# Kernel tuning notes

Measured on AMD Instinct MI355X. Metric: run time of the kernel, lower is better.

Reference implementation:

```python
import jax, jax.numpy as jnp
import numpy as np

N = 50000        # num_nodes
E = 800000       # num edges (avg degree 16)
IN = 512         # embedding_dim[0]
H = 128          # hidden_dim = embedding_dim[1]
C = 64           # out_dim = n_classes = embedding_dim[-1]
L = 3            # layer_num = len(embedding_dim) - 1


def _lin(k, fan_in, fan_out):
    s = 1.0 / np.sqrt(fan_in)
    k1, k2 = jax.random.split(k)
    W = jax.random.uniform(k1, (fan_in, fan_out), jnp.float32, -s, s)
    b = jax.random.uniform(k2, (fan_out,), jnp.float32, -s, s)
    return W, b


def setup_inputs() -> dict:
    key = jax.random.key(0)
    ks = jax.random.split(key, 12)
    d = {}
    d["x"] = jax.random.normal(ks[0], (N, IN), jnp.float32)
    d["edge_index"] = jax.random.randint(ks[1], (2, E), 0, N)
    # pseudo_mlp: in_dim -> 512 -> 64 -> out_dim
    d["Wp1"], d["bp1"] = _lin(ks[2], IN, 512)
    d["Wp2"], d["bp2"] = _lin(ks[3], 512, 64)
    d["Wp3"], d["bp3"] = _lin(ks[4], 64, C)
    # parsing_mats[0] (only ln=0 is used in learn_soft_edge3), init ones/scaling_factor
    d["parsing0"] = jnp.ones((C, C), jnp.float32) / 2.0 + 0.01 * jax.random.normal(ks[5], (C, C), jnp.float32)
    # GCNConv weights (PyG style: linear without bias, bias added after aggregation)
    d["Wg0"], d["bg0"] = _lin(ks[6], IN, H)
    d["Wg1"], d["bg1"] = _lin(ks[7], H, H)
    d["Wg2"], d["bg2"] = _lin(ks[8], H, H)
    # JK 'cat' -> lin1 input is (layer_num-1)*hidden
    d["Wl1"], d["bl1"] = _lin(ks[9], (L - 1) * H, H)
    d["Wl2"], d["bl2"] = _lin(ks[10], H, C)
    return d


def gcn_conv(x, W, b, edge_index, ew, n):
    """PyG GCNConv with per-edge weight ew, add_self_loops=True (loop weight 1)."""
    xw = x @ W                                           # [N, F_out]
    row, col = edge_index[0], edge_index[1]
    loop = jnp.arange(n)
    row2 = jnp.concatenate([row, loop])
    col2 = jnp.concatenate([col, loop])
    ew2 = jnp.concatenate([ew, jnp.ones((n,), xw.dtype)])
    deg = jax.ops.segment_sum(ew2, col2, num_segments=n)
    dis = jnp.where(deg > 0, jax.lax.rsqrt(deg), 0.0)    # deg^-1/2, inf -> 0
    norm = dis[row2] * ew2 * dis[col2]                   # [E+N]
    out = jax.ops.segment_sum(norm[:, None] * xw[row2], col2, num_segments=n)
    return out + b


def soft_edge_weight(x, edge_index, Wp1, bp1, Wp2, bp2, Wp3, bp3, parsing0):
    """learn_soft_edge3: bilinear form start^T * relu(2*P) * end per edge.
    Original materializes an [E,C,C] outer product then bmm + diagonal; the
    diagonal-sum equals einsum('ek,ed,dk->e', start, end, parsing), computed
    here as a fused small matmul + elementwise reduce (same math)."""
    h = jax.nn.relu(x @ Wp1 + bp1)
    h = jax.nn.relu(h @ Wp2 + bp2)
    logits = h @ Wp3 + bp3                               # [N, C]
    parsing = jax.nn.relu(2.0 * parsing0)                # scaling_factor = 2
    s = logits[edge_index[0]]                            # [E, C] start
    e = logits[edge_index[1]]                            # [E, C] end
    ew = jnp.sum((e @ parsing) * s, axis=-1)             # [E]
    mean = ew.mean()
    var = jnp.var(ew, ddof=1)                            # torch .var() is unbiased
    return (ew - mean) * jnp.sqrt(1e-4 / var) + 1.0


def reference(x, edge_index, Wp1, bp1, Wp2, bp2, Wp3, bp3, parsing0,
              Wg0, bg0, Wg1, bg1, Wg2, bg2, Wl1, bl1, Wl2, bl2):
    n = x.shape[0]
    ew = soft_edge_weight(x, edge_index, Wp1, bp1, Wp2, bp2, Wp3, bp3, parsing0)
    # layer 0
    x1 = jax.nn.relu(gcn_conv(x, Wg0, bg0, edge_index, ew, n))
    xs = [x1]
    # ln = 1 (not last): conv -> relu -> (dropout off in eval) -> append
    x2 = jax.nn.relu(gcn_conv(x1, Wg1, bg1, edge_index, ew, n))
    xs.append(x2)
    # ln = 2 (last layer): computed in original but loop breaks before append;
    # jump(xs) overwrites x, so the last conv's output never reaches the output.
    xj = jnp.concatenate(xs, axis=-1)                    # JK 'cat' -> [N, (L-1)*H]
    out = jax.nn.relu(xj @ Wl1 + bl1)
    out = out @ Wl2 + bl2                                # [N, C]
    return out
```

## Files before the change

### kernel.cpp

```cpp
#include <hip/hip_runtime.h>
#include <hip/hip_bf16.h>
#include <cmath>
#include <cstring>

#define NNODES 50000
#define NEDGES 800000
#define IND    512
#define HD     128
#define CD     64

typedef __bf16 bf16x8 __attribute__((ext_vector_type(8)));
typedef float  f32x4  __attribute__((ext_vector_type(4)));
typedef const __attribute__((address_space(1))) unsigned int* gu32p;
typedef __attribute__((address_space(3))) unsigned int* lu32p;

static const size_t XJ_B   = 0;
static const size_t HID_B  = 25600000;
static const size_t H1_B   = 51200000;
static const size_t XW_B   = 102400000;
static const size_t H2_B   = 115200000;
static const size_t LG_B   = 121600000;
static const size_t PE_B   = 128000000;
static const size_t WT_B   = 134400000;
static const size_t CSRR_B = 135300000;
static const size_t EWC_B  = 138500000;
static const size_t CSRW_B = 141700000;
static const size_t CNT_B  = 144900000;
static const size_t S_B    = 145100000;
static const size_t ZERO_BYTES = 200016;
static const size_t RP_B   = 145100016;
static const size_t WOFF_B = 145300020;
static const size_t INCL_B = 145500020;
static const size_t BSUM_B = 145700020;
static const size_t ST_B   = 145701044;
static const size_t DIS_B  = 145701052;

static const size_t WP1T_O = 0;
static const size_t WG0T_O = 524288;
static const size_t WP2T_O = 655360;
static const size_t WP3T_O = 720896;
static const size_t W2T_O  = 729088;
static const size_t WG1T_O = 737280;
static const size_t WL1T_O = 770048;
static const size_t WL2T_O = 835584;
static const size_t BG1_O  = 851968;
static const size_t BG3_O  = 854528;

struct WD { const float* s; __hip_bfloat16* d; int K; int N; };
struct PrepArgs {
    const float* x; __hip_bfloat16* xb;
    WD w[7];
    int bo[8];
    const float* Wp3; const float* bp3; const float* P0; const float* bp1;
    __hip_bfloat16* W2t; float* bias_g1; float* bias_g3;
};
#define PREP_CAST_BLKS 12500
#define PREP_TP_BLKS   1648
#define PREP_BLKS      (PREP_CAST_BLKS + PREP_TP_BLKS + 20)

__global__ __launch_bounds__(256) void prep_all(PrepArgs a)
{
    int b = blockIdx.x;
    int t = threadIdx.x;
    if (b < PREP_CAST_BLKS) {
        int i = b * 256 + t;
        const float4* p = (const float4*)a.x + (size_t)i * 2;
        float4 u = p[0], v = p[1];
        __hip_bfloat16 o[8] __attribute__((aligned(16)));
        o[0] = __float2bfloat16(u.x); o[1] = __float2bfloat16(u.y);
        o[2] = __float2bfloat16(u.z); o[3] = __float2bfloat16(u.w);
        o[4] = __float2bfloat16(v.x); o[5] = __float2bfloat16(v.y);
        o[6] = __float2bfloat16(v.z); o[7] = __float2bfloat16(v.w);
        *(int4*)(a.xb + (size_t)i * 8) = *(const int4*)o;
        return;
    }
    b -= PREP_CAST_BLKS;
    if (b < PREP_TP_BLKS) {
        int m = 0;
        #pragma unroll
        for (int q = 1; q < 7; q++) if (b >= a.bo[q]) m = q;
        WD d = a.w[m];
        int i = (b - a.bo[m]) * 256 + t;
        if (i < d.K * d.N) {
            int k = i % d.K, n = i / d.K;
            d.d[i] = __float2bfloat16(d.s[(size_t)k * d.N + n]);
        }
        return;
    }
    b -= PREP_TP_BLKS;
    if (b < 16) {
        int i = b * 256 + t;
        int k = i >> 6, n = i & 63;
        float s = 0.f;
        for (int j = 0; j < 64; j++)
            s += a.Wp3[k * 64 + j] * fmaxf(2.f * a.P0[j * 64 + n], 0.f);
        a.W2t[n * 64 + k] = __float2bfloat16(s);
    } else if (b == 16) {
        int n = t;
        if (n < 64) {
            float s = 0.f;
            for (int j = 0; j < 64; j++)
                s += a.bp3[j] * fmaxf(2.f * a.P0[j * 64 + n], 0.f);
            a.bias_g3[n] = a.bp3[n];
            a.bias_g3[64 + n] = s;
        }
    } else {
        int i = (b - 17) * 256 + t;
        if (i < 512) a.bias_g1[i] = a.bp1[i];
        else if (i < 640) a.bias_g1[i] = 0.f;
    }
}

template<int BM, int BN, int WN>
__global__ __launch_bounds__(256) void gemm_mfma(
    const __hip_bfloat16* __restrict__ Ab, int lda,
    const __hip_bfloat16* __restrict__ Bt, int ldb,
    const float* __restrict__ bias,
    void* __restrict__ Cout, int ldc,
    void* __restrict__ Cout2, int ldc2, int splitN,
    int M, int K, int do_relu, int out_bf16)
{
    constexpr int BF = WN / 16;
    constexpr int MI = BM / 32;
    constexpr int APASS = BM / 64;
    constexpr int BPASS = BN / 64;
    __shared__ __bf16 As[2][BM * 32];
    __shared__ __bf16 Bs[2][BN * 32];

    const int NC = gridDim.x, NR = gridDim.y;
    int g = blockIdx.y * NC + blockIdx.x;
    int per = NC * 8;
    int nfull = (NR >> 3) * per;
    int rowt, colt;
    if (g < nfull) {
        int grp = g / per, rem = g % per;
        rowt = grp * 8 + (rem & 7);
        colt = rem >> 3;
    } else {
        int rem = g - nfull;
        int tail = NR - (NR >> 3) * 8;
        rowt = (NR >> 3) * 8 + rem % tail;
        colt = rem / tail;
    }

    const int t = threadIdx.x;
    const int row0 = rowt * BM;
    const int col0 = colt * BN;

    const int wv   = t >> 6;
    const int lane = t & 63;
    const int quad = lane >> 4;
    const int l16  = lane & 15;
    const int wrow = (wv >> 1) * (BM / 2);
    const int wcol = (wv & 1) * WN;

    const int subrow = lane >> 2;
    const int kchunk = (lane & 3) ^ (subrow & 3);
    const int subkg  = kchunk * 8;

    f32x4 acc[MI][BF] = {};

    for (int k0 = 0; k0 < K; k0 += 64) {
        #pragma unroll
        for (int h = 0; h < 2; h++) {
            int kh = k0 + h * 32;
            #pragma unroll
            for (int p = 0; p < APASS; p++) {
                int rowA = (p * 4 + wv) * 16 + subrow;
                const __hip_bfloat16* gp = Ab + (size_t)(row0 + rowA) * lda + kh + subkg;
                __builtin_amdgcn_global_load_lds((gu32p)(const void*)gp,
                    (lu32p)(void*)&As[h][(p * 4 + wv) * 512], 16, 0, 0);
            }
            #pragma unroll
            for (int p = 0; p < BPASS; p++) {
                int rowB = (p * 4 + wv) * 16 + subrow;
                const __hip_bfloat16* gp = Bt + (size_t)(col0 + rowB) * ldb + kh + subkg;
                __builtin_amdgcn_global_load_lds((gu32p)(const void*)gp,
                    (lu32p)(void*)&Bs[h][(p * 4 + wv) * 512], 16, 0, 0);
            }
        }
        __syncthreads();

        #pragma unroll
        for (int h = 0; h < 2; h++) {
            bf16x8 af[MI], bfr[BF];
            #pragma unroll
            for (int i = 0; i < MI; i++) {
                int R = wrow + i * 16 + l16;
                af[i] = *(const bf16x8*)&As[h][R * 32 + ((quad ^ (R & 3)) * 8)];
            }
            #pragma unroll
            for (int j = 0; j < BF; j++) {
                int R = wcol + j * 16 + l16;
                bfr[j] = *(const bf16x8*)&Bs[h][R * 32 + ((quad ^ (R & 3)) * 8)];
            }
            #pragma unroll
            for (int i = 0; i < MI; i++)
                #pragma unroll
                for (int j = 0; j < BF; j++)
                    acc[i][j] = __builtin_amdgcn_mfma_f32_16x16x32_bf16(af[i], bfr[j], acc[i][j], 0, 0, 0);
        }
        if (k0 + 64 < K) __syncthreads();
    }

    #pragma unroll
    for (int i = 0; i < MI; i++) {
        #pragma unroll
        for (int j = 0; j < BF; j++) {
            int n = col0 + wcol + j * 16 + l16;
            bool second = (n >= splitN);
            float bv = bias ? bias[n] : 0.f;
            #pragma unroll
            for (int reg = 0; reg < 4; reg++) {
                int m = row0 + wrow + i * 16 + quad * 4 + reg;
                if (m >= M) continue;
                float v = acc[i][j][reg] + bv;
                if (do_relu && !second) v = fmaxf(v, 0.f);
                if (second)
                    ((__hip_bfloat16*)Cout2)[(size_t)m * ldc2 + (n - splitN)] = __float2bfloat16(v);
                else if (out_bf16)
                    ((__hip_bfloat16*)Cout)[(size_t)m * ldc + n] = __float2bfloat16(v);
                else
                    ((float*)Cout)[(size_t)m * ldc + n] = v;
            }
        }
    }
}

template<int BN1, int WN1, int N2, int SPLIT2, int OUT2F32>
__global__ __launch_bounds__(256) void gemm_fused(
    const __hip_bfloat16* __restrict__ Ab, int lda,
    const __hip_bfloat16* __restrict__ B1t, int ldb1,
    const float* __restrict__ bias1,
    const __hip_bfloat16* __restrict__ B2t,
    const float* __restrict__ bias2,
    void* __restrict__ Out1, int ldo1,
    void* __restrict__ Out2, int ldo2,
    int M, int K1)
{
    constexpr int BF1 = WN1 / 16;
    constexpr int BPASS1 = BN1 / 64;
    constexpr int K2H = BN1 / 32;
    constexpr int WN2 = N2 / 2;
    constexpr int BF2 = WN2 / 16;
    constexpr int P2 = N2 / 64;
    __shared__ __bf16 L1[4096 + BN1 * 64];
    __shared__ __bf16 Bs2[8192];

    const int t = threadIdx.x;
    const int row0 = blockIdx.y * 64;
    const int wv   = t >> 6;
    const int lane = t & 63;
    const int quad = lane >> 4;
    const int l16  = lane & 15;
    const int wrow1 = (wv >> 1) * 32;
    const int wcol1 = (wv & 1) * WN1;
    const int subrow = lane >> 2;
    const int subkg  = ((lane & 3) ^ (subrow & 3)) * 8;

    #pragma unroll
    for (int hh = 0; hh < K2H; hh++)
        #pragma unroll
        for (int p = 0; p < P2; p++) {
            int rowB = (p * 4 + wv) * 16 + subrow;
            const __hip_bfloat16* gp = B2t + (size_t)rowB * BN1 + hh * 32 + subkg;
            __builtin_amdgcn_global_load_lds((gu32p)(const void*)gp,
                (lu32p)(void*)&Bs2[hh * (N2 * 32) + (p * 4 + wv) * 512], 16, 0, 0);
        }

    f32x4 acc1[2][BF1] = {};
    for (int k0 = 0; k0 < K1; k0 += 64) {
        #pragma unroll
        for (int h = 0; h < 2; h++) {
            int kh = k0 + h * 32;
            {
                int rowA = wv * 16 + subrow;
                const __hip_bfloat16* gp = Ab + (size_t)(row0 + rowA) * lda + kh + subkg;
                __builtin_amdgcn_global_load_lds((gu32p)(const void*)gp,
                    (lu32p)(void*)&L1[h * 2048 + wv * 512], 16, 0, 0);
            }
            #pragma unroll
            for (int p = 0; p < BPASS1; p++) {
                int rowB = (p * 4 + wv) * 16 + subrow;
                const __hip_bfloat16* gp = B1t + (size_t)rowB * ldb1 + kh + subkg;
                __builtin_amdgcn_global_load_lds((gu32p)(const void*)gp,
                    (lu32p)(void*)&L1[4096 + h * (BN1 * 32) + (p * 4 + wv) * 512], 16, 0, 0);
            }
        }
        __syncthreads();
        #pragma unroll
        for (int h = 0; h < 2; h++) {
            bf16x8 af[2], bfr[BF1];
            #pragma unroll
            for (int i = 0; i < 2; i++) {
                int R = wrow1 + i * 16 + l16;
                af[i] = *(const bf16x8*)&L1[h * 2048 + R * 32 + ((quad ^ (R & 3)) * 8)];
            }
            #pragma unroll
            for (int j = 0; j < BF1; j++) {
                int R = wcol1 + j * 16 + l16;
                bfr[j] = *(const bf16x8*)&L1[4096 + h * (BN1 * 32) + R * 32 + ((quad ^ (R & 3)) * 8)];
            }
            #pragma unroll
            for (int i = 0; i < 2; i++)
                #pragma unroll
                for (int j = 0; j < BF1; j++)
                    acc1[i][j] = __builtin_amdgcn_mfma_f32_16x16x32_bf16(af[i], bfr[j], acc1[i][j], 0, 0, 0);
        }
        __syncthreads();
    }

    #pragma unroll
    for (int i = 0; i < 2; i++)
        #pragma unroll
        for (int j = 0; j < BF1; j++) {
            int n1 = wcol1 + j * 16 + l16;
            float bv = bias1[n1];
            int h = n1 >> 5, kk = n1 & 31;
            int q = kk >> 3, pp = kk & 7;
            #pragma unroll
            for (int reg = 0; reg < 4; reg++) {
                int r = wrow1 + i * 16 + quad * 4 + reg;
                float v = fmaxf(acc1[i][j][reg] + bv, 0.f);
                __hip_bfloat16 hb = __float2bfloat16(v);
                unsigned short us; memcpy(&us, &hb, 2);
                *(unsigned short*)&L1[h * 2048 + r * 32 + ((q ^ (r & 3)) * 8) + pp] = us;
            }
        }
    __syncthreads();

    const int wrow2 = (wv >> 1) * 32;
    const int wcol2 = (wv & 1) * WN2;
    f32x4 acc2[2][BF2] = {};
    #pragma unroll
    for (int hh = 0; hh < K2H; hh++) {
        bf16x8 af2[2], bf2[BF2];
        #pragma unroll
        for (int i = 0; i < 2; i++) {
            int R = wrow2 + i * 16 + l16;
            af2[i] = *(const bf16x8*)&L1[hh * 2048 + R * 32 + ((quad ^ (R & 3)) * 8)];
        }
        #pragma unroll
        for (int j = 0; j < BF2; j++) {
            int R = wcol2 + j * 16 + l16;
            bf2[j] = *(const bf16x8*)&Bs2[hh * (N2 * 32) + R * 32 + ((quad ^ (R & 3)) * 8)];
        }
        #pragma unroll
        for (int i = 0; i < 2; i++)
            #pragma unroll
            for (int j = 0; j < BF2; j++)
                acc2[i][j] = __builtin_amdgcn_mfma_f32_16x16x32_bf16(af2[i], bf2[j], acc2[i][j], 0, 0, 0);
    }

    #pragma unroll
    for (int i = 0; i < 2; i++)
        #pragma unroll
        for (int j = 0; j < BF2; j++) {
            int n2 = wcol2 + j * 16 + l16;
            float bv = bias2[n2];
            #pragma unroll
            for (int reg = 0; reg < 4; reg++) {
                int m = row0 + wrow2 + i * 16 + quad * 4 + reg;
                if (m >= M) continue;
                float v = acc2[i][j][reg] + bv;
                if (SPLIT2) {
                    if (n2 < 64)
                        ((__hip_bfloat16*)Out1)[(size_t)m * ldo1 + n2] = __float2bfloat16(v);
                    else
                        ((__hip_bfloat16*)Out2)[(size_t)m * ldo2 + (n2 - 64)] = __float2bfloat16(v);
                } else if (OUT2F32) {
                    ((float*)Out1)[(size_t)m * ldo1 + n2] = v;
                } else {
                    ((__hip_bfloat16*)Out1)[(size_t)m * ldo1 + n2] = __float2bfloat16(v);
                }
            }
        }
}

__global__ __launch_bounds__(256) void count_kernel(
    const int* __restrict__ ei, int* __restrict__ cnt)
{
    int e = blockIdx.x * 256 + threadIdx.x;
    if (e >= NEDGES) return;
    atomicAdd(&cnt[ei[NEDGES + e]], 1);
}

__global__ __launch_bounds__(256) void scan1_kernel(
    const int* __restrict__ cnt, int* __restrict__ incl, int* __restrict__ bsum)
{
    __shared__ int s[256];
    int t = threadIdx.x;
    int i = blockIdx.x * 256 + t;
    int v = (i < NNODES) ? cnt[i] : 0;
    s[t] = v;
    __syncthreads();
    for (int off = 1; off < 256; off <<= 1) {
        int u = (t >= off) ? s[t - off] : 0;
        __syncthreads();
        s[t] += u;
        __syncthreads();
    }
    if (i < NNODES) incl[i] = s[t];
    if (t == 255) bsum[blockIdx.x] = s[255];
}

__global__ __launch_bounds__(256) void scan3_kernel(
    const int* __restrict__ cnt, const int* __restrict__ incl,
    const int* __restrict__ bsum, int* __restrict__ rowptr,
    int* __restrict__ woff, int nb)
{
    __shared__ int s[256];
    int t = threadIdx.x;
    int v = (t < nb) ? bsum[t] : 0;
    s[t] = v;
    __syncthreads();
    for (int off = 1; off < 256; off <<= 1) {
        int u = (t >= off) ? s[t - off] : 0;
        __syncthreads();
        s[t] += u;
        __syncthreads();
    }
    int off = s[blockIdx.x] - bsum[blockIdx.x];
    int i = blockIdx.x * 256 + t;
    if (i >= NNODES) return;
    int r = incl[i] - cnt[i] + off;
    rowptr[i] = r;
    woff[i] = r;
    if (i == NNODES - 1) rowptr[NNODES] = incl[i] + off;
}

__global__ __launch_bounds__(256) void scatter_idx_kernel(
    const int* __restrict__ ei, int* __restrict__ woff,
    int* __restrict__ csr_row, int* __restrict__ csr_col)
{
    int e = blockIdx.x * 256 + threadIdx.x;
    if (e >= NEDGES) return;
    int r = ei[e];
    int c = ei[NEDGES + e];
    int p = atomicAdd(&woff[c], 1);
    csr_row[p] = r;
    csr_col[p] = c;
}

__global__ __launch_bounds__(256) void edge_ew_gather(
    const __hip_bfloat16* __restrict__ lg, const __hip_bfloat16* __restrict__ pe,
    const int* __restrict__ csr_row, const int* __restrict__ csr_col,
    float* __restrict__ ew_csr)
{
    const int tid = threadIdx.x;
    const int sub = tid & 7;
    const int e = blockIdx.x * 32 + (tid >> 3);
    if (e >= NEDGES) return;
    int r = csr_row[e];
    int c = csr_col[e];
    bf16x8 a = *(const bf16x8*)(lg + (size_t)r * CD + sub * 8);
    bf16x8 b = *(const bf16x8*)(pe + (size_t)c * CD + sub * 8);
    float acc = 0.f;
    #pragma unroll
    for (int u = 0; u < 8; u++)
        acc += (float)a[u] * (float)b[u];
    acc += __shfl_xor(acc, 1);
    acc += __shfl_xor(acc, 2);
    acc += __shfl_xor(acc, 4);
    if (sub == 0) ew_csr[e] = acc;
}

__global__ __launch_bounds__(256) void ew_stats_kernel(
    const float* __restrict__ ew, double* __restrict__ S)
{
    const int tid = threadIdx.x;
    double s1 = 0.0, s2 = 0.0;
    for (int i = blockIdx.x * 256 + tid; i < NEDGES; i += gridDim.x * 256) {
        float v = ew[i];
        s1 += v; s2 += (double)v * (double)v;
    }
    __shared__ double sh1[256], sh2[256];
    sh1[tid] = s1; sh2[tid] = s2;
    __syncthreads();
    for (int s = 128; s > 0; s >>= 1) {
        if (tid < s) { sh1[tid] += sh1[tid + s]; sh2[tid] += sh2[tid + s]; }
        __syncthreads();
    }
    if (tid == 0) {
        atomicAdd(&S[0], sh1[0]);
        atomicAdd(&S[1], sh2[0]);
    }
}

__global__ __launch_bounds__(256) void norm_deg_kernel(
    const int* __restrict__ rowptr, float* __restrict__ ew_csr,
    const double* __restrict__ S, float* __restrict__ dis)
{
    int n = blockIdx.x * 256 + threadIdx.x;
    if (n >= NNODES) return;
    const double Ed = (double)NEDGES;
    double meand = S[0] / Ed;
    double var = (S[1] - S[0] * S[0] / Ed) / (Ed - 1.0);
    float mean = (float)meand;
    float alpha = (float)sqrt(1e-4 / var);
    int s = rowptr[n], e = rowptr[n + 1];
    float sum = 0.f;
    for (int j = s; j < e; j++) {
        float w = (ew_csr[j] - mean) * alpha + 1.0f;
        ew_csr[j] = w;
        sum += w;
    }
    float d = sum + 1.0f;
    dis[n] = (d > 0.f) ? rsqrtf(d) : 0.f;
}

__global__ __launch_bounds__(256) void csrw_kernel(
    const int* __restrict__ rowptr, const int* __restrict__ csr_row,
    const float* __restrict__ ew_csr, const float* __restrict__ dis,
    float* __restrict__ csr_w)
{
    int n = blockIdx.x * 256 + threadIdx.x;
    if (n >= NNODES) return;
    float dn = dis[n];
    int s = rowptr[n], e = rowptr[n + 1];
    for (int j = s; j < e; j++)
        csr_w[j] = dis[csr_row[j]] * ew_csr[j] * dn;
}

__global__ __launch_bounds__(128) void agg_kernel(
    const unsigned* __restrict__ xw32, const float* __restrict__ dis,
    const int* __restrict__ rowptr, const int* __restrict__ csr_row,
    const float* __restrict__ csr_w, const float* __restrict__ bias,
    __hip_bfloat16* __restrict__ out, int ldo)
{
    const int wv = threadIdx.x >> 6, lane = threadIdx.x & 63;
    const int n = blockIdx.x * 2 + wv;
    if (n >= NNODES) return;
    float dn = dis[n];
    unsigned v0 = xw32[(size_t)n * 64 + lane];
    float aL = dn * dn * __uint_as_float(v0 << 16);
    float aH = dn * dn * __uint_as_float(v0 & 0xffff0000u);
    int s = rowptr[n], e = rowptr[n + 1];
    int j = s;
    for (; j + 4 <= e; j += 4) {
        int r0 = csr_row[j], r1 = csr_row[j + 1];
        int r2 = csr_row[j + 2], r3 = csr_row[j + 3];
        float w0 = csr_w[j], w1 = csr_w[j + 1];
        float w2 = csr_w[j + 2], w3 = csr_w[j + 3];
        unsigned g0 = xw32[(size_t)r0 * 64 + lane];
        unsigned g1 = xw32[(size_t)r1 * 64 + lane];
        unsigned g2 = xw32[(size_t)r2 * 64 + lane];
        unsigned g3 = xw32[(size_t)r3 * 64 + lane];
        aL = fmaf(w0, __uint_as_float(g0 << 16), aL);
        aH = fmaf(w0, __uint_as_float(g0 & 0xffff0000u), aH);
        aL = fmaf(w1, __uint_as_float(g1 << 16), aL);
        aH = fmaf(w1, __uint_as_float(g1 & 0xffff0000u), aH);
        aL = fmaf(w2, __uint_as_float(g2 << 16), aL);
        aH = fmaf(w2, __uint_as_float(g2 & 0xffff0000u), aH);
        aL = fmaf(w3, __uint_as_float(g3 << 16), aL);
        aH = fmaf(w3, __uint_as_float(g3 & 0xffff0000u), aH);
    }
    for (; j < e; j++) {
        int r = csr_row[j];
        float w = csr_w[j];
        unsigned g = xw32[(size_t)r * 64 + lane];
        aL = fmaf(w, __uint_as_float(g << 16), aL);
        aH = fmaf(w, __uint_as_float(g & 0xffff0000u), aH);
    }
    float2 b = *(const float2*)(bias + 2 * lane);
    aL = fmaxf(aL + b.x, 0.f);
    aH = fmaxf(aH + b.y, 0.f);
    __hip_bfloat16 bl = __float2bfloat16(aL), bh = __float2bfloat16(aH);
    unsigned short ul, uh;
    memcpy(&ul, &bl, 2); memcpy(&uh, &bh, 2);
    unsigned o = (unsigned)ul | ((unsigned)uh << 16);
    *(unsigned*)(out + (size_t)n * ldo + 2 * lane) = o;
}

extern "C" void kernel_launch(void* const* d_in, const int* in_sizes, int n_in,
                              void* d_out, int out_size, void* d_ws, size_t ws_size,
                              hipStream_t stream)
{
    const float* x   = (const float*)d_in[0];
    const int*   ei  = (const int*)d_in[1];
    const float* Wp1 = (const float*)d_in[2];
    const float* bp1 = (const float*)d_in[3];
    const float* Wp2 = (const float*)d_in[4];
    const float* bp2 = (const float*)d_in[5];
    const float* Wp3 = (const float*)d_in[6];
    const float* bp3 = (const float*)d_in[7];
    const float* P0  = (const float*)d_in[8];
    const float* Wg0 = (const float*)d_in[9];
    const float* bg0 = (const float*)d_in[10];
    const float* Wg1 = (const float*)d_in[11];
    const float* bg1 = (const float*)d_in[12];
    const float* Wl1 = (const float*)d_in[15];
    const float* bl1 = (const float*)d_in[16];
    const float* Wl2 = (const float*)d_in[17];
    const float* bl2 = (const float*)d_in[18];
    float* out = (float*)d_out;

    char* wsb = (char*)d_ws;
    __hip_bfloat16* xj     = (__hip_bfloat16*)(wsb + XJ_B);
    __hip_bfloat16* xb16   = (__hip_bfloat16*)(wsb + XJ_B);
    __hip_bfloat16* h1     = (__hip_bfloat16*)(wsb + H1_B);
    __hip_bfloat16* xw     = (__hip_bfloat16*)(wsb + XW_B);
    __hip_bfloat16* lg     = (__hip_bfloat16*)(wsb + LG_B);
    __hip_bfloat16* pe     = (__hip_bfloat16*)(wsb + PE_B);
    int*            csr_row= (int*)(wsb + CSRR_B);
    float*          ew_csr = (float*)(wsb + EWC_B);
    int*            csr_col= (int*)(wsb + CSRW_B);
    float*          csr_w  = (float*)(wsb + CSRW_B);
    int*            cnt    = (int*)(wsb + CNT_B);
    double*         S      = (double*)(wsb + S_B);
    int*            rowptr = (int*)(wsb + RP_B);
    int*            woff   = (int*)(wsb + WOFF_B);
    int*            incl   = (int*)(wsb + INCL_B);
    int*            bsum   = (int*)(wsb + BSUM_B);
    float*          dis    = (float*)(wsb + DIS_B);

    __hip_bfloat16* Wp1t = (__hip_bfloat16*)(wsb + WT_B + WP1T_O);
    __hip_bfloat16* Wg0t = (__hip_bfloat16*)(wsb + WT_B + WG0T_O);
    __hip_bfloat16* Wp2t = (__hip_bfloat16*)(wsb + WT_B + WP2T_O);
    __hip_bfloat16* Wp3t = (__hip_bfloat16*)(wsb + WT_B + WP3T_O);
    __hip_bfloat16* W2t  = (__hip_bfloat16*)(wsb + WT_B + W2T_O);
    __hip_bfloat16* Wg1t = (__hip_bfloat16*)(wsb + WT_B + WG1T_O);
    __hip_bfloat16* Wl1t = (__hip_bfloat16*)(wsb + WT_B + WL1T_O);
    __hip_bfloat16* Wl2t = (__hip_bfloat16*)(wsb + WT_B + WL2T_O);
    float*          bias_g1 = (float*)(wsb + WT_B + BG1_O);
    float*          bias_g3 = (float*)(wsb + WT_B + BG3_O);

    const int EB = (NEDGES + 255) / 256;
    const int NB = (NNODES + 255) / 256;
    const int MT  = (NNODES + 127) / 128;
    const int MT64 = (NNODES + 63) / 64;
    const int BIGN = 1 << 30;

    hipMemsetAsync(wsb + CNT_B, 0, ZERO_BYTES, stream);

    PrepArgs pa;
    pa.x = x; pa.xb = xb16;
    pa.w[0] = { Wp1, Wp1t, 512, 512 };
    pa.w[1] = { Wg0, Wg0t, 512, 128 };
    pa.w[2] = { Wp2, Wp2t, 512,  64 };
    pa.w[3] = { Wp3, Wp3t,  64,  64 };
    pa.w[4] = { Wg1, Wg1t, 128, 128 };
    pa.w[5] = { Wl1, Wl1t, 256, 128 };
    pa.w[6] = { Wl2, Wl2t, 128,  64 };
    pa.bo[0] = 0;    pa.bo[1] = 1024; pa.bo[2] = 1280; pa.bo[3] = 1408;
    pa.bo[4] = 1424; pa.bo[5] = 1488; pa.bo[6] = 1616; pa.bo[7] = 1648;
    pa.Wp3 = Wp3; pa.bp3 = bp3; pa.P0 = P0; pa.bp1 = bp1;
    pa.W2t = W2t; pa.bias_g1 = bias_g1; pa.bias_g3 = bias_g3;
    prep_all<<<PREP_BLKS, 256, 0, stream>>>(pa);

    count_kernel<<<EB, 256, 0, stream>>>(ei, cnt);
    scan1_kernel<<<NB, 256, 0, stream>>>(cnt, incl, bsum);
    scan3_kernel<<<NB, 256, 0, stream>>>(cnt, incl, bsum, rowptr, woff, NB);
    scatter_idx_kernel<<<EB, 256, 0, stream>>>(ei, woff, csr_row, csr_col);

    gemm_mfma<128, 128, 64><<<dim3(5, MT), 256, 0, stream>>>(
        xb16, 512, Wp1t, 512, bias_g1, h1, 512, xw, 128, 512, NNODES, 512, 1, 1);

    gemm_fused<64, 32, 128, 1, 0><<<dim3(1, MT64), 256, 0, stream>>>(
        h1, 512, Wp2t, 512, bp2, Wp3t, bias_g3, lg, 64, pe, 64, NNODES, 512);

    edge_ew_gather<<<(NEDGES + 31) / 32, 256, 0, stream>>>(lg, pe, csr_row, csr_col, ew_csr);
    ew_stats_kernel<<<512, 256, 0, stream>>>(ew_csr, S);
    norm_deg_kernel<<<NB, 256, 0, stream>>>(rowptr, ew_csr, S, dis);
    csrw_kernel<<<NB, 256, 0, stream>>>(rowptr, csr_row, ew_csr, dis, csr_w);

    agg_kernel<<<25000, 128, 0, stream>>>((const unsigned*)xw, dis, rowptr, csr_row, csr_w, bg0, xj, 2 * HD);

    gemm_mfma<64, 64, 32><<<dim3(2, MT64), 256, 0, stream>>>(
        xj, 2 * HD, Wg1t, 128, nullptr, xw, 128, nullptr, 0, BIGN, NNODES, 128, 0, 1);
    agg_kernel<<<25000, 128, 0, stream>>>((const unsigned*)xw, dis, rowptr, csr_row, csr_w, bg1, xj + HD, 2 * HD);

    gemm_fused<128, 64, 64, 0, 1><<<dim3(1, MT64), 256, 0, stream>>>(
        xj, 2 * HD, Wl1t, 256, bl1, Wl2t, bl2, out, 64, nullptr, 0, NNODES, 256);
}
```

Measured before the change: 523.2 us.

## Fuse edge counting into prep and edge-weight stats into gather; retile first GEMM

The edge in-degree counting moves into the prep_all launch as extra blocks, and the sum and sum-of-squares reduction for edge-weight normalization moves into edge_ew_gather through wavefront shuffles and per-block atomics. Two separate kernel launches and a re-read of ew_csr go away. The first big GEMM switches from 128x128 to 128x64 tiles with twice as many column blocks, which changes occupancy and reuse. The gather now issues one double atomic pair per block (25000 blocks), which may cause atomic contention, and it drops its bounds check because E divides evenly by 32.

```diff
diff --git a/kernel.cpp b/kernel.cpp
--- a/kernel.cpp
+++ b/kernel.cpp
@@ -32,7 +32,6 @@
 static const size_t WOFF_B = 145300020;
 static const size_t INCL_B = 145500020;
 static const size_t BSUM_B = 145700020;
-static const size_t ST_B   = 145701044;
 static const size_t DIS_B  = 145701052;
 
 static const size_t WP1T_O = 0;
@@ -53,10 +52,13 @@
     int bo[8];
     const float* Wp3; const float* bp3; const float* P0; const float* bp1;
     __hip_bfloat16* W2t; float* bias_g1; float* bias_g3;
+    const int* ei; int* cnt;
 };
-#define PREP_CAST_BLKS 12500
-#define PREP_TP_BLKS   1648
-#define PREP_BLKS      (PREP_CAST_BLKS + PREP_TP_BLKS + 20)
+#define PREP_CAST_BLKS  12500
+#define PREP_TP_BLKS    1648
+#define PREP_CMB_BLKS   20
+#define PREP_CNT_BLKS   3125
+#define PREP_BLKS (PREP_CAST_BLKS + PREP_TP_BLKS + PREP_CMB_BLKS + PREP_CNT_BLKS)
 
 __global__ __launch_bounds__(256) void prep_all(PrepArgs a)
 {
@@ -88,27 +90,33 @@
         return;
     }
     b -= PREP_TP_BLKS;
-    if (b < 16) {
-        int i = b * 256 + t;
-        int k = i >> 6, n = i & 63;
-        float s = 0.f;
-        for (int j = 0; j < 64; j++)
-            s += a.Wp3[k * 64 + j] * fmaxf(2.f * a.P0[j * 64 + n], 0.f);
-        a.W2t[n * 64 + k] = __float2bfloat16(s);
-    } else if (b == 16) {
-        int n = t;
-        if (n < 64) {
+    if (b < PREP_CMB_BLKS) {
+        if (b < 16) {
+            int i = b * 256 + t;
+            int k = i >> 6, n = i & 63;
             float s = 0.f;
             for (int j = 0; j < 64; j++)
-                s += a.bp3[j] * fmaxf(2.f * a.P0[j * 64 + n], 0.f);
-            a.bias_g3[n] = a.bp3[n];
-            a.bias_g3[64 + n] = s;
-        }
-    } else {
-        int i = (b - 17) * 256 + t;
-        if (i < 512) a.bias_g1[i] = a.bp1[i];
-        else if (i < 640) a.bias_g1[i] = 0.f;
-    }
+                s += a.Wp3[k * 64 + j] * fmaxf(2.f * a.P0[j * 64 + n], 0.f);
+            a.W2t[n * 64 + k] = __float2bfloat16(s);
+        } else if (b == 16) {
+            int n = t;
+            if (n < 64) {
+                float s = 0.f;
+                for (int j = 0; j < 64; j++)
+                    s += a.bp3[j] * fmaxf(2.f * a.P0[j * 64 + n], 0.f);
+                a.bias_g3[n] = a.bp3[n];
+                a.bias_g3[64 + n] = s;
+            }
+        } else {
+            int i = (b - 17) * 256 + t;
+            if (i < 512) a.bias_g1[i] = a.bp1[i];
+            else if (i < 640) a.bias_g1[i] = 0.f;
+        }
+        return;
+    }
+    b -= PREP_CMB_BLKS;
+    int e = b * 256 + t;
+    atomicAdd(&a.cnt[a.ei[NEDGES + e]], 1);
 }
 
 template<int BM, int BN, int WN>
@@ -377,14 +385,6 @@
         }
 }
 
-__global__ __launch_bounds__(256) void count_kernel(
-    const int* __restrict__ ei, int* __restrict__ cnt)
-{
-    int e = blockIdx.x * 256 + threadIdx.x;
-    if (e >= NEDGES) return;
-    atomicAdd(&cnt[ei[NEDGES + e]], 1);
-}
-
 __global__ __launch_bounds__(256) void scan1_kernel(
     const int* __restrict__ cnt, int* __restrict__ incl, int* __restrict__ bsum)
 {
@@ -445,12 +445,11 @@
 __global__ __launch_bounds__(256) void edge_ew_gather(
     const __hip_bfloat16* __restrict__ lg, const __hip_bfloat16* __restrict__ pe,
     const int* __restrict__ csr_row, const int* __restrict__ csr_col,
-    float* __restrict__ ew_csr)
+    float* __restrict__ ew_csr, double* __restrict__ S)
 {
     const int tid = threadIdx.x;
     const int sub = tid & 7;
     const int e = blockIdx.x * 32 + (tid >> 3);
-    if (e >= NEDGES) return;
     int r = csr_row[e];
     int c = csr_col[e];
     bf16x8 a = *(const bf16x8*)(lg + (size_t)r * CD + sub * 8);
@@ -463,27 +462,20 @@
     acc += __shfl_xor(acc, 2);
     acc += __shfl_xor(acc, 4);
     if (sub == 0) ew_csr[e] = acc;
-}
-
-__global__ __launch_bounds__(256) void ew_stats_kernel(
-    const float* __restrict__ ew, double* __restrict__ S)
-{
-    const int tid = threadIdx.x;
-    double s1 = 0.0, s2 = 0.0;
-    for (int i = blockIdx.x * 256 + tid; i < NEDGES; i += gridDim.x * 256) {
-        float v = ew[i];
-        s1 += v; s2 += (double)v * (double)v;
-    }
-    __shared__ double sh1[256], sh2[256];
-    sh1[tid] = s1; sh2[tid] = s2;
+
+    double s1 = (sub == 0) ? (double)acc : 0.0;
+    double s2 = (sub == 0) ? (double)acc * (double)acc : 0.0;
+    #pragma unroll
+    for (int off = 8; off < 64; off <<= 1) {
+        s1 += __shfl_xor(s1, off);
+        s2 += __shfl_xor(s2, off);
+    }
+    __shared__ double sh1[4], sh2[4];
+    if ((tid & 63) == 0) { sh1[tid >> 6] = s1; sh2[tid >> 6] = s2; }
     __syncthreads();
-    for (int s = 128; s > 0; s >>= 1) {
-        if (tid < s) { sh1[tid] += sh1[tid + s]; sh2[tid] += sh2[tid + s]; }
-        __syncthreads();
-    }
     if (tid == 0) {
-        atomicAdd(&S[0], sh1[0]);
-        atomicAdd(&S[1], sh2[0]);
+        atomicAdd(&S[0], sh1[0] + sh1[1] + sh1[2] + sh1[3]);
+        atomicAdd(&S[1], sh2[0] + sh2[1] + sh2[2] + sh2[3]);
     }
 }
 
@@ -646,21 +638,20 @@
     pa.bo[4] = 1424; pa.bo[5] = 1488; pa.bo[6] = 1616; pa.bo[7] = 1648;
     pa.Wp3 = Wp3; pa.bp3 = bp3; pa.P0 = P0; pa.bp1 = bp1;
     pa.W2t = W2t; pa.bias_g1 = bias_g1; pa.bias_g3 = bias_g3;
+    pa.ei = ei; pa.cnt = cnt;
     prep_all<<<PREP_BLKS, 256, 0, stream>>>(pa);
 
-    count_kernel<<<EB, 256, 0, stream>>>(ei, cnt);
     scan1_kernel<<<NB, 256, 0, stream>>>(cnt, incl, bsum);
     scan3_kernel<<<NB, 256, 0, stream>>>(cnt, incl, bsum, rowptr, woff, NB);
     scatter_idx_kernel<<<EB, 256, 0, stream>>>(ei, woff, csr_row, csr_col);
 
-    gemm_mfma<128, 128, 64><<<dim3(5, MT), 256, 0, stream>>>(
+    gemm_mfma<128, 64, 32><<<dim3(10, MT), 256, 0, stream>>>(
         xb16, 512, Wp1t, 512, bias_g1, h1, 512, xw, 128, 512, NNODES, 512, 1, 1);
 
     gemm_fused<64, 32, 128, 1, 0><<<dim3(1, MT64), 256, 0, stream>>>(
         h1, 512, Wp2t, 512, bp2, Wp3t, bias_g3, lg, 64, pe, 64, NNODES, 512);
 
-    edge_ew_gather<<<(NEDGES + 31) / 32, 256, 0, stream>>>(lg, pe, csr_row, csr_col, ew_csr);
-    ew_stats_kernel<<<512, 256, 0, stream>>>(ew_csr, S);
+    edge_ew_gather<<<NEDGES / 32, 256, 0, stream>>>(lg, pe, csr_row, csr_col, ew_csr, S);
     norm_deg_kernel<<<NB, 256, 0, stream>>>(rowptr, ew_csr, S, dis);
     csrw_kernel<<<NB, 256, 0, stream>>>(rowptr, csr_row, ew_csr, dis, csr_w);
 
```

Result: slower. 1.082 ms (+106.7%).
